# Performance work log

Measured on AMD Instinct MI355X. Metric: run time of the kernel, lower is better.

## Reference

```python
import jax, jax.numpy as jnp
import numpy as np

HIDDEN = 100
N_NODE = 100000
B = 512
T = 50

def setup_inputs() -> dict:
    key = jax.random.key(0)
    ks = jax.random.split(key, 20)
    stdv = 1.0 / np.sqrt(HIDDEN)
    u = lambda k, shape: jax.random.uniform(k, shape, jnp.float32, -stdv, stdv)
    d = HIDDEN
    return {
        "adj_in": jax.random.uniform(ks[0], (B, T, T), jnp.float32),
        "adj_out": jax.random.uniform(ks[1], (B, T, T), jnp.float32),
        "mask": jnp.ones((B, T), jnp.float32),
        "item": jax.random.randint(ks[2], (B, T), 0, N_NODE, jnp.int32),
        "alias": jax.random.randint(ks[3], (B, T), 0, T, jnp.int32),
        "step": 1,
        "embedding": u(ks[4], (N_NODE, d)),
        "W_in": u(ks[5], (d, d)),
        "b_in": u(ks[6], (d,)),
        "W_out": u(ks[7], (d, d)),
        "b_out": u(ks[8], (d,)),
        "gru_gate_k": u(ks[9], (3 * d, 2 * d)),
        "gru_gate_b": jnp.ones((2 * d,), jnp.float32),  # TF GRUCell gate bias init = 1.0
        "gru_cand_k": u(ks[10], (3 * d, d)),
        "gru_cand_b": jnp.zeros((d,), jnp.float32),
        "nasr_w1": u(ks[11], (d, d)),
        "nasr_w2": u(ks[12], (d, d)),
        "nasr_v": u(ks[13], (1, d)),
        "nasr_b": jnp.zeros((d,), jnp.float32),
        "B_mat": u(ks[14], (2 * d, d)),
    }


def _ggnn(item, adj_in, adj_out, embedding, W_in, b_in, W_out, b_out,
          gru_gate_k, gru_gate_b, gru_cand_k, gru_cand_b, step):
    h = embedding[item]  # [B,T,d]
    d = h.shape[-1]
    for _ in range(step):
        a_in = jnp.einsum('bts,bsd->btd', adj_in, h @ W_in + b_in)
        a_out = jnp.einsum('bts,bsd->btd', adj_out, h @ W_out + b_out)
        a = jnp.concatenate([a_in, a_out], axis=-1)  # [B,T,2d]
        # TF GRUCell: gates then candidate
        gates = jax.nn.sigmoid(jnp.concatenate([a, h], -1) @ gru_gate_k + gru_gate_b)
        r, u_ = gates[..., :d], gates[..., d:]
        c = jnp.tanh(jnp.concatenate([a, r * h], -1) @ gru_cand_k + gru_cand_b)
        h = u_ * h + (1.0 - u_) * c
    return h  # [B,T,d]


def reference(adj_in, adj_out, mask, item, alias, step, embedding,
              W_in, b_in, W_out, b_out, gru_gate_k, gru_gate_b,
              gru_cand_k, gru_cand_b, nasr_w1, nasr_w2, nasr_v, nasr_b, B_mat):
    d = embedding.shape[1]
    re_emb = _ggnn(item, adj_in, adj_out, embedding, W_in, b_in, W_out, b_out,
                   gru_gate_k, gru_gate_b, gru_cand_k, gru_cand_b, step)
    rm = jnp.sum(jax.lax.stop_gradient(mask), axis=1)  # session lengths
    bidx = jnp.arange(re_emb.shape[0])
    last_id = alias[bidx, rm.astype(jnp.int32) - 1]          # [B]
    last_h = re_emb[bidx, last_id]                            # [B,d]
    seq_h = jnp.take_along_axis(re_emb, alias[..., None], axis=1)  # [B,L,d]
    last = last_h @ nasr_w1                                   # [B,d]
    seq = seq_h @ nasr_w2                                     # [B,L,d]
    m = jax.nn.sigmoid(last[:, None, :] + seq + nasr_b)       # [B,L,d]
    coef = (m @ nasr_v[0]) * mask                             # [B,L]
    ma = jnp.concatenate([jnp.sum(coef[..., None] * seq_h, axis=1), last], axis=-1)  # [B,2d]
    y1 = ma @ B_mat                                           # [B,d]
    logits = y1 @ embedding[1:].T                             # [B,n_node-1]
    return logits
```

## Files before the change

### kernel.cpp

```cpp
#include <hip/hip_runtime.h>
#include <math.h>

#define D 100
#define T 50
#define BB 512
#define NOUT 99999

__device__ __forceinline__ float sigf(float x) { return 1.f / (1.f + expf(-x)); }

__global__ __launch_bounds__(256) void ggnn_fused(
    const float* __restrict__ adj_in, const float* __restrict__ adj_out,
    const float* __restrict__ mask,   const int* __restrict__ item,
    const int* __restrict__ alias_,   const float* __restrict__ emb,
    const float* __restrict__ W_in,   const float* __restrict__ b_in,
    const float* __restrict__ W_out,  const float* __restrict__ b_out,
    const float* __restrict__ gate_k, const float* __restrict__ gate_b,
    const float* __restrict__ cand_k, const float* __restrict__ cand_b,
    const float* __restrict__ w1,     const float* __restrict__ w2,
    const float* __restrict__ v,      const float* __restrict__ nb,
    const float* __restrict__ Bm,     float* __restrict__ y1)
{
    __shared__ float hS[T*D];
    __shared__ float R1[T*D];
    __shared__ float R2[T*D];
    __shared__ float maskS[T+2], vS[D], nbS[D], lastWS[D], coefS[T+2], maS[2*D];
    __shared__ int aliasS[T+2];
    __shared__ int rmidx;

    const int b = blockIdx.x, tid = threadIdx.x;
    const size_t bT = (size_t)b * T;

    if (tid < T) {
        aliasS[tid] = alias_[bT + tid];
        maskS[tid]  = mask[bT + tid];
    }
    if (tid >= 64 && tid < 64 + D) {
        int k = tid - 64;
        vS[k] = v[k]; nbS[k] = nb[k];
    }
    for (int idx = tid; idx < T*25; idx += 256) {
        int t = idx / 25, q = idx - t*25;
        int node = item[bT + t];
        *(float4*)&hS[t*D + q*4] = *(const float4*)&emb[(size_t)node*D + q*4];
    }
    __syncthreads();
    if (tid == 0) {
        float s = 0.f;
        for (int t = 0; t < T; ++t) s += maskS[t];
        rmidx = aliasS[(int)s - 1];
    }

    const bool act250 = tid < 250;
    const int tg50  = tid / 50;
    const int rem50 = tid % 50;
    const int cg25  = tid / 25;
    const int jq25  = tid % 25;

    if (act250) {
        const int which = rem50 / 25, jq = rem50 % 25;
        const int t0 = tg50 * 10;
        const float* W  = which ? W_out : W_in;
        const float* bb = which ? b_out : b_in;
        float4 binit = *(const float4*)&bb[jq*4];
        float4 acc[10];
        #pragma unroll
        for (int tt = 0; tt < 10; ++tt) acc[tt] = binit;
        for (int k = 0; k < D; k += 2) {
            float4 wa = *(const float4*)&W[k*D + jq*4];
            float4 wb = *(const float4*)&W[(k+1)*D + jq*4];
            #pragma unroll
            for (int tt = 0; tt < 10; ++tt) {
                float2 a = *(const float2*)&hS[(t0+tt)*D + k];
                acc[tt].x += a.x*wa.x + a.y*wb.x;
                acc[tt].y += a.x*wa.y + a.y*wb.y;
                acc[tt].z += a.x*wa.z + a.y*wb.z;
                acc[tt].w += a.x*wa.w + a.y*wb.w;
            }
        }
        float* dst = which ? R2 : R1;
        #pragma unroll
        for (int tt = 0; tt < 10; ++tt)
            *(float4*)&dst[(t0+tt)*D + jq*4] = acc[tt];
    }
    __syncthreads();

    float4 eacc[10];
    if (act250) {
        const int which = rem50 / 25, jq = rem50 % 25;
        const int t0 = tg50 * 10;
        const float* adj = which ? adj_out : adj_in;
        const float* Xs  = which ? R2 : R1;
        #pragma unroll
        for (int tt = 0; tt < 10; ++tt) eacc[tt] = make_float4(0.f,0.f,0.f,0.f);
        #pragma unroll 2
        for (int s = 0; s < T; ++s) {
            float4 x = *(const float4*)&Xs[s*D + jq*4];
            const float* ap = &adj[(bT + t0)*T + s];
            #pragma unroll
            for (int tt = 0; tt < 10; ++tt) {
                float a = ap[tt*T];
                eacc[tt].x += a*x.x; eacc[tt].y += a*x.y;
                eacc[tt].z += a*x.z; eacc[tt].w += a*x.w;
            }
        }
    }
    __syncthreads();
    if (act250) {
        const int which = rem50 / 25, jq = rem50 % 25;
        const int t0 = tg50 * 10;
        float* dst = which ? R2 : R1;
        #pragma unroll
        for (int tt = 0; tt < 10; ++tt)
            *(float4*)&dst[(t0+tt)*D + jq*4] = eacc[tt];
    }
    __syncthreads();

    float4 gacc[10];
    if (act250) {
        const int nq = rem50;
        const int t0 = tg50 * 10;
        float4 ginit = *(const float4*)&gate_b[nq*4];
        #pragma unroll
        for (int tt = 0; tt < 10; ++tt) gacc[tt] = ginit;
        for (int k = 0; k < D; k += 2) {
            float4 g0a = *(const float4*)&gate_k[(size_t)k*200 + nq*4];
            float4 g0b = *(const float4*)&gate_k[(size_t)(k+1)*200 + nq*4];
            float4 g1a = *(const float4*)&gate_k[(size_t)(k+100)*200 + nq*4];
            float4 g1b = *(const float4*)&gate_k[(size_t)(k+101)*200 + nq*4];
            float4 g2a = *(const float4*)&gate_k[(size_t)(k+200)*200 + nq*4];
            float4 g2b = *(const float4*)&gate_k[(size_t)(k+201)*200 + nq*4];
            #pragma unroll
            for (int tt = 0; tt < 10; ++tt) {
                float2 a0 = *(const float2*)&R1[(t0+tt)*D + k];
                float2 a1 = *(const float2*)&R2[(t0+tt)*D + k];
                float2 a2 = *(const float2*)&hS[(t0+tt)*D + k];
                gacc[tt].x += a0.x*g0a.x + a0.y*g0b.x + a1.x*g1a.x + a1.y*g1b.x + a2.x*g2a.x + a2.y*g2b.x;
                gacc[tt].y += a0.x*g0a.y + a0.y*g0b.y + a1.x*g1a.y + a1.y*g1b.y + a2.x*g2a.y + a2.y*g2b.y;
                gacc[tt].z += a0.x*g0a.z + a0.y*g0b.z + a1.x*g1a.z + a1.y*g1b.z + a2.x*g2a.z + a2.y*g2b.z;
                gacc[tt].w += a0.x*g0a.w + a0.y*g0b.w + a1.x*g1a.w + a1.y*g1b.w + a2.x*g2a.w + a2.y*g2b.w;
            }
        }
        #pragma unroll
        for (int tt = 0; tt < 10; ++tt) {
            gacc[tt].x = sigf(gacc[tt].x); gacc[tt].y = sigf(gacc[tt].y);
            gacc[tt].z = sigf(gacc[tt].z); gacc[tt].w = sigf(gacc[tt].w);
        }
    }

    float4 cacc[5];
    if (act250) {
        const int t0 = cg25 * 5;
        float4 cinit = *(const float4*)&cand_b[jq25*4];
        #pragma unroll
        for (int tt = 0; tt < 5; ++tt) cacc[tt] = cinit;
        for (int k = 0; k < D; k += 2) {
            float4 c0a = *(const float4*)&cand_k[(size_t)k*D + jq25*4];
            float4 c0b = *(const float4*)&cand_k[(size_t)(k+1)*D + jq25*4];
            float4 c1a = *(const float4*)&cand_k[(size_t)(k+100)*D + jq25*4];
            float4 c1b = *(const float4*)&cand_k[(size_t)(k+101)*D + jq25*4];
            #pragma unroll
            for (int tt = 0; tt < 5; ++tt) {
                float2 a0 = *(const float2*)&R1[(t0+tt)*D + k];
                float2 a1 = *(const float2*)&R2[(t0+tt)*D + k];
                cacc[tt].x += a0.x*c0a.x + a0.y*c0b.x + a1.x*c1a.x + a1.y*c1b.x;
                cacc[tt].y += a0.x*c0a.y + a0.y*c0b.y + a1.x*c1a.y + a1.y*c1b.y;
                cacc[tt].z += a0.x*c0a.z + a0.y*c0b.z + a1.x*c1a.z + a1.y*c1b.z;
                cacc[tt].w += a0.x*c0a.w + a0.y*c0b.w + a1.x*c1a.w + a1.y*c1b.w;
            }
        }
    }
    __syncthreads();

    if (act250) {
        const int nq = rem50;
        const int t0 = tg50 * 10;
        if (nq < 25) {
            #pragma unroll
            for (int tt = 0; tt < 10; ++tt) {
                float4 hh = *(const float4*)&hS[(t0+tt)*D + nq*4];
                float4 g = gacc[tt];
                float4 o; o.x = g.x*hh.x; o.y = g.y*hh.y; o.z = g.z*hh.z; o.w = g.w*hh.w;
                *(float4*)&R1[(t0+tt)*D + nq*4] = o;
            }
        } else {
            #pragma unroll
            for (int tt = 0; tt < 10; ++tt)
                *(float4*)&R2[(t0+tt)*D + (nq-25)*4] = gacc[tt];
        }
    }
    __syncthreads();

    if (act250) {
        const int t0 = cg25 * 5;
        for (int k = 0; k < D; k += 2) {
            float4 c2a = *(const float4*)&cand_k[(size_t)(k+200)*D + jq25*4];
            float4 c2b = *(const float4*)&cand_k[(size_t)(k+201)*D + jq25*4];
            #pragma unroll
            for (int tt = 0; tt < 5; ++tt) {
                float2 rh = *(const float2*)&R1[(t0+tt)*D + k];
                cacc[tt].x += rh.x*c2a.x + rh.y*c2b.x;
                cacc[tt].y += rh.x*c2a.y + rh.y*c2b.y;
                cacc[tt].z += rh.x*c2a.z + rh.y*c2b.z;
                cacc[tt].w += rh.x*c2a.w + rh.y*c2b.w;
            }
        }
        #pragma unroll
        for (int tt = 0; tt < 5; ++tt) {
            float4 c4;
            c4.x = tanhf(cacc[tt].x); c4.y = tanhf(cacc[tt].y);
            c4.z = tanhf(cacc[tt].z); c4.w = tanhf(cacc[tt].w);
            float4 u4 = *(const float4*)&R2[(t0+tt)*D + jq25*4];
            float4 hh = *(const float4*)&hS[(t0+tt)*D + jq25*4];
            float4 o;
            o.x = u4.x*hh.x + (1.f-u4.x)*c4.x;
            o.y = u4.y*hh.y + (1.f-u4.y)*c4.y;
            o.z = u4.z*hh.z + (1.f-u4.z)*c4.z;
            o.w = u4.w*hh.w + (1.f-u4.w)*c4.w;
            *(float4*)&hS[(t0+tt)*D + jq25*4] = o;
        }
    }
    __syncthreads();

    if (tid < 125) {
        const int sg = tid / 25, jq = tid % 25;
        const int t0 = sg * 10;
        float4 sacc[10];
        #pragma unroll
        for (int tt = 0; tt < 10; ++tt) sacc[tt] = make_float4(0.f,0.f,0.f,0.f);
        int at[10];
        #pragma unroll
        for (int tt = 0; tt < 10; ++tt) at[tt] = aliasS[t0+tt];
        for (int k = 0; k < D; k += 2) {
            float4 wa = *(const float4*)&w2[(size_t)k*D + jq*4];
            float4 wb = *(const float4*)&w2[(size_t)(k+1)*D + jq*4];
            #pragma unroll
            for (int tt = 0; tt < 10; ++tt) {
                float2 a = *(const float2*)&hS[at[tt]*D + k];
                sacc[tt].x += a.x*wa.x + a.y*wb.x;
                sacc[tt].y += a.x*wa.y + a.y*wb.y;
                sacc[tt].z += a.x*wa.z + a.y*wb.z;
                sacc[tt].w += a.x*wa.w + a.y*wb.w;
            }
        }
        #pragma unroll
        for (int tt = 0; tt < 10; ++tt)
            *(float4*)&R1[(t0+tt)*D + jq*4] = sacc[tt];
    } else if (tid >= 128 && tid < 153) {
        const int jq = tid - 128;
        const int lid = rmidx;
        float4 acc = make_float4(0.f,0.f,0.f,0.f);
        for (int k = 0; k < D; k += 2) {
            float4 wa = *(const float4*)&w1[(size_t)k*D + jq*4];
            float4 wb = *(const float4*)&w1[(size_t)(k+1)*D + jq*4];
            float2 a = *(const float2*)&hS[lid*D + k];
            acc.x += a.x*wa.x + a.y*wb.x;
            acc.y += a.x*wa.y + a.y*wb.y;
            acc.z += a.x*wa.z + a.y*wb.z;
            acc.w += a.x*wa.w + a.y*wb.w;
        }
        *(float4*)&lastWS[jq*4] = acc;
    }
    __syncthreads();

    if (tid < T) {
        float s = 0.f;
        #pragma unroll 4
        for (int k = 0; k < D; ++k) {
            float x = lastWS[k] + R1[tid*D + k] + nbS[k];
            s += vS[k] * sigf(x);
        }
        coefS[tid] = s * maskS[tid];
    }
    __syncthreads();
    if (tid < 25) {
        float4 acc = make_float4(0.f,0.f,0.f,0.f);
        #pragma unroll 5
        for (int t = 0; t < T; ++t) {
            float c = coefS[t];
            float4 hh = *(const float4*)&hS[aliasS[t]*D + tid*4];
            acc.x += c*hh.x; acc.y += c*hh.y; acc.z += c*hh.z; acc.w += c*hh.w;
        }
        *(float4*)&maS[tid*4] = acc;
    } else if (tid >= 32 && tid < 57) {
        int j4 = tid - 32;
        *(float4*)&maS[D + j4*4] = *(const float4*)&lastWS[j4*4];
    }
    __syncthreads();
    if (tid < 25) {
        float4 acc = make_float4(0.f,0.f,0.f,0.f);
        #pragma unroll 4
        for (int k = 0; k < 2*D; ++k) {
            float a = maS[k];
            float4 w = *(const float4*)&Bm[(size_t)k*D + tid*4];
            acc.x += a*w.x; acc.y += a*w.y; acc.z += a*w.z; acc.w += a*w.w;
        }
        *(float4*)&y1[(size_t)b*D + tid*4] = acc;
    }
}

#define LDB 132

#define GB_COMPUTE(Ab, kbase) do {                                            \
    _Pragma("unroll")                                                         \
    for (int kk = 0; kk < 4; ++kk) {                                          \
        float bq[8];                                                          \
        _Pragma("unroll")                                                     \
        for (int j = 0; j < 8; ++j)                                           \
            bq[j] = Bs[(kbase + kk)*LDB + (j>>2)*64 + (j&3)*16 + tx];         \
        _Pragma("unroll")                                                     \
        for (int i = 0; i < 8; ++i) {                                         \
            float a_ = kk==0 ? Ab[i].x : kk==1 ? Ab[i].y :                    \
                       kk==2 ? Ab[i].z : Ab[i].w;                             \
            _Pragma("unroll")                                                 \
            for (int j = 0; j < 8; ++j)                                       \
                acc[i][j] += a_ * bq[j];                                      \
        }                                                                     \
    }                                                                         \
} while (0)

__global__ __launch_bounds__(256) void gemm_big(
    const float* __restrict__ y1,
    const float* __restrict__ emb,
    float* __restrict__ out)
{
    __shared__ float Bs[100*LDB];
    const int tid = threadIdx.x;
    const int tx = tid & 15, ty = tid >> 4;
    const int n0 = blockIdx.x * 128;

    for (int idx = tid; idx < 128*25; idx += 256) {
        int n = idx / 25, q = idx - n*25;
        int gn = n0 + n;
        float4 vv = make_float4(0.f,0.f,0.f,0.f);
        if (gn < NOUT) vv = *(const float4*)&emb[(size_t)(gn+1)*D + q*4];
        Bs[(q*4+0)*LDB + n] = vv.x;
        Bs[(q*4+1)*LDB + n] = vv.y;
        Bs[(q*4+2)*LDB + n] = vv.z;
        Bs[(q*4+3)*LDB + n] = vv.w;
    }
    __syncthreads();

    float acc[8][8];
    float4 A0[8], A1[8];

    #pragma unroll 1
    for (int mc = 0; mc < 2; ++mc) {
        const int m0 = blockIdx.y * 256 + mc * 128;

        #pragma unroll
        for (int i = 0; i < 8; ++i)
            #pragma unroll
            for (int j = 0; j < 8; ++j) acc[i][j] = 0.f;

        #pragma unroll
        for (int i = 0; i < 8; ++i)
            A0[i] = *(const float4*)&y1[(size_t)(m0 + ty + i*16)*D + 0];

        int k = 0;
        #pragma unroll 1
        for (int it = 0; it < 12; ++it, k += 8) {
            #pragma unroll
            for (int i = 0; i < 8; ++i)
                A1[i] = *(const float4*)&y1[(size_t)(m0 + ty + i*16)*D + k + 4];
            GB_COMPUTE(A0, k);
            #pragma unroll
            for (int i = 0; i < 8; ++i)
                A0[i] = *(const float4*)&y1[(size_t)(m0 + ty + i*16)*D + k + 8];
            GB_COMPUTE(A1, k + 4);
        }
        GB_COMPUTE(A0, 96);

        #pragma unroll
        for (int i = 0; i < 8; ++i) {
            size_t row = (size_t)(m0 + ty + i*16) * NOUT;
            #pragma unroll
            for (int h = 0; h < 2; ++h)
                #pragma unroll
                for (int q = 0; q < 4; ++q) {
                    int n = n0 + h*64 + q*16 + tx;
                    if (n < NOUT) out[row + n] = acc[i][h*4+q];
                }
        }
    }
}

extern "C" void kernel_launch(void* const* d_in, const int* in_sizes, int n_in,
                              void* d_out, int out_size, void* d_ws, size_t ws_size,
                              hipStream_t stream)
{
    const float* adj_in  = (const float*)d_in[0];
    const float* adj_out = (const float*)d_in[1];
    const float* mask    = (const float*)d_in[2];
    const int*   item    = (const int*)  d_in[3];
    const int*   alias_  = (const int*)  d_in[4];
    const float* emb     = (const float*)d_in[6];
    const float* W_in    = (const float*)d_in[7];
    const float* b_in    = (const float*)d_in[8];
    const float* W_out   = (const float*)d_in[9];
    const float* b_out   = (const float*)d_in[10];
    const float* gate_k  = (const float*)d_in[11];
    const float* gate_b  = (const float*)d_in[12];
    const float* cand_k  = (const float*)d_in[13];
    const float* cand_b  = (const float*)d_in[14];
    const float* w1      = (const float*)d_in[15];
    const float* w2      = (const float*)d_in[16];
    const float* v       = (const float*)d_in[17];
    const float* nb      = (const float*)d_in[18];
    const float* Bm      = (const float*)d_in[19];
    float* out = (float*)d_out;
    float* y1  = (float*)d_ws;

    ggnn_fused<<<BB, 256, 0, stream>>>(
        adj_in, adj_out, mask, item, alias_, emb,
        W_in, b_in, W_out, b_out, gate_k, gate_b, cand_k, cand_b,
        w1, w2, v, nb, Bm, y1);

    gemm_big<<<dim3((NOUT + 127)/128, 2), 256, 0, stream>>>(y1, emb, out);
}
```

Measured before the change: 646.9 us.

## Software-pipeline weight loads in GGNN matmuls and vectorize big-GEMM shared reads

```diff
diff --git a/kernel.cpp b/kernel.cpp
--- a/kernel.cpp
+++ b/kernel.cpp
@@ -65,18 +65,28 @@
         float4 acc[10];
         #pragma unroll
         for (int tt = 0; tt < 10; ++tt) acc[tt] = binit;
-        for (int k = 0; k < D; k += 2) {
-            float4 wa = *(const float4*)&W[k*D + jq*4];
-            float4 wb = *(const float4*)&W[(k+1)*D + jq*4];
-            #pragma unroll
-            for (int tt = 0; tt < 10; ++tt) {
-                float2 a = *(const float2*)&hS[(t0+tt)*D + k];
-                acc[tt].x += a.x*wa.x + a.y*wb.x;
-                acc[tt].y += a.x*wa.y + a.y*wb.y;
-                acc[tt].z += a.x*wa.z + a.y*wb.z;
-                acc[tt].w += a.x*wa.w + a.y*wb.w;
-            }
-        }
+
+        float4 wq[4], wp[4];
+#define P2_LOAD(dst, k0) { _Pragma("unroll") \
+        for (int d = 0; d < 4; ++d) dst[d] = *(const float4*)&W[((k0)+d)*D + jq*4]; }
+#define P2_COMP(buf, k0) { _Pragma("unroll") \
+        for (int d2 = 0; d2 < 4; d2 += 2) { _Pragma("unroll") \
+            for (int tt = 0; tt < 10; ++tt) { \
+                float2 a = *(const float2*)&hS[(t0+tt)*D + (k0) + d2]; \
+                acc[tt].x += a.x*buf[d2].x + a.y*buf[d2+1].x; \
+                acc[tt].y += a.x*buf[d2].y + a.y*buf[d2+1].y; \
+                acc[tt].z += a.x*buf[d2].z + a.y*buf[d2+1].z; \
+                acc[tt].w += a.x*buf[d2].w + a.y*buf[d2+1].w; } } }
+        P2_LOAD(wq, 0);
+        #pragma unroll 1
+        for (int k = 0; k < 88; k += 8) {
+            P2_LOAD(wp, k+4);  P2_COMP(wq, k);
+            P2_LOAD(wq, k+8);  P2_COMP(wp, k+4);
+        }
+        P2_LOAD(wp, 92);  P2_COMP(wq, 88);
+        P2_LOAD(wq, 96);  P2_COMP(wp, 92);
+        P2_COMP(wq, 96);
+
         float* dst = which ? R2 : R1;
         #pragma unroll
         for (int tt = 0; tt < 10; ++tt)
@@ -88,20 +98,32 @@
     if (act250) {
         const int which = rem50 / 25, jq = rem50 % 25;
         const int t0 = tg50 * 10;
-        const float* adj = which ? adj_out : adj_in;
-        const float* Xs  = which ? R2 : R1;
-        #pragma unroll
-        for (int tt = 0; tt < 10; ++tt) eacc[tt] = make_float4(0.f,0.f,0.f,0.f);
-        #pragma unroll 2
-        for (int s = 0; s < T; ++s) {
+        const float* adjp = which ? adj_out : adj_in;
+        const float* Xs   = which ? R2 : R1;
+        const float* apb  = &adjp[(bT + t0)*T];
+        float ac[10], an[10];
+        #pragma unroll
+        for (int tt = 0; tt < 10; ++tt) {
+            eacc[tt] = make_float4(0.f,0.f,0.f,0.f);
+            ac[tt] = apb[tt*T];
+        }
+        #pragma unroll 1
+        for (int s = 0; s < T-1; ++s) {
+            #pragma unroll
+            for (int tt = 0; tt < 10; ++tt) an[tt] = apb[tt*T + s + 1];
             float4 x = *(const float4*)&Xs[s*D + jq*4];
-            const float* ap = &adj[(bT + t0)*T + s];
             #pragma unroll
             for (int tt = 0; tt < 10; ++tt) {
-                float a = ap[tt*T];
-                eacc[tt].x += a*x.x; eacc[tt].y += a*x.y;
-                eacc[tt].z += a*x.z; eacc[tt].w += a*x.w;
+                eacc[tt].x += ac[tt]*x.x; eacc[tt].y += ac[tt]*x.y;
+                eacc[tt].z += ac[tt]*x.z; eacc[tt].w += ac[tt]*x.w;
+                ac[tt] = an[tt];
             }
+        }
+        float4 x = *(const float4*)&Xs[(T-1)*D + jq*4];
+        #pragma unroll
+        for (int tt = 0; tt < 10; ++tt) {
+            eacc[tt].x += ac[tt]*x.x; eacc[tt].y += ac[tt]*x.y;
+            eacc[tt].z += ac[tt]*x.z; eacc[tt].w += ac[tt]*x.w;
         }
     }
     __syncthreads();
@@ -122,24 +144,31 @@
         float4 ginit = *(const float4*)&gate_b[nq*4];
         #pragma unroll
         for (int tt = 0; tt < 10; ++tt) gacc[tt] = ginit;
-        for (int k = 0; k < D; k += 2) {
-            float4 g0a = *(const float4*)&gate_k[(size_t)k*200 + nq*4];
-            float4 g0b = *(const float4*)&gate_k[(size_t)(k+1)*200 + nq*4];
-            float4 g1a = *(const float4*)&gate_k[(size_t)(k+100)*200 + nq*4];
-            float4 g1b = *(const float4*)&gate_k[(size_t)(k+101)*200 + nq*4];
-            float4 g2a = *(const float4*)&gate_k[(size_t)(k+200)*200 + nq*4];
-            float4 g2b = *(const float4*)&gate_k[(size_t)(k+201)*200 + nq*4];
-            #pragma unroll
-            for (int tt = 0; tt < 10; ++tt) {
-                float2 a0 = *(const float2*)&R1[(t0+tt)*D + k];
-                float2 a1 = *(const float2*)&R2[(t0+tt)*D + k];
-                float2 a2 = *(const float2*)&hS[(t0+tt)*D + k];
-                gacc[tt].x += a0.x*g0a.x + a0.y*g0b.x + a1.x*g1a.x + a1.y*g1b.x + a2.x*g2a.x + a2.y*g2b.x;
-                gacc[tt].y += a0.x*g0a.y + a0.y*g0b.y + a1.x*g1a.y + a1.y*g1b.y + a2.x*g2a.y + a2.y*g2b.y;
-                gacc[tt].z += a0.x*g0a.z + a0.y*g0b.z + a1.x*g1a.z + a1.y*g1b.z + a2.x*g2a.z + a2.y*g2b.z;
-                gacc[tt].w += a0.x*g0a.w + a0.y*g0b.w + a1.x*g1a.w + a1.y*g1b.w + a2.x*g2a.w + a2.y*g2b.w;
-            }
-        }
+
+        float4 gq6[6], gp6[6];
+#define P4_LOAD(dst, kp) { _Pragma("unroll") \
+        for (int s = 0; s < 3; ++s) { \
+            dst[s*2]   = *(const float4*)&gate_k[(size_t)((kp)+s*100)*200 + nq*4]; \
+            dst[s*2+1] = *(const float4*)&gate_k[(size_t)((kp)+1+s*100)*200 + nq*4]; } }
+#define P4_COMP(buf, kp) { _Pragma("unroll") \
+        for (int tt = 0; tt < 10; ++tt) { \
+            float2 a0 = *(const float2*)&R1[(t0+tt)*D + (kp)]; \
+            float2 a1 = *(const float2*)&R2[(t0+tt)*D + (kp)]; \
+            float2 a2 = *(const float2*)&hS[(t0+tt)*D + (kp)]; \
+            gacc[tt].x += a0.x*buf[0].x + a0.y*buf[1].x + a1.x*buf[2].x + a1.y*buf[3].x + a2.x*buf[4].x + a2.y*buf[5].x; \
+            gacc[tt].y += a0.x*buf[0].y + a0.y*buf[1].y + a1.x*buf[2].y + a1.y*buf[3].y + a2.x*buf[4].y + a2.y*buf[5].y; \
+            gacc[tt].z += a0.x*buf[0].z + a0.y*buf[1].z + a1.x*buf[2].z + a1.y*buf[3].z + a2.x*buf[4].z + a2.y*buf[5].z; \
+            gacc[tt].w += a0.x*buf[0].w + a0.y*buf[1].w + a1.x*buf[2].w + a1.y*buf[3].w + a2.x*buf[4].w + a2.y*buf[5].w; } }
+        P4_LOAD(gq6, 0);
+        #pragma unroll 1
+        for (int k = 0; k < 96; k += 4) {
+            P4_LOAD(gp6, k+2);  P4_COMP(gq6, k);
+            P4_LOAD(gq6, k+4);  P4_COMP(gp6, k+2);
+        }
+        P4_LOAD(gp6, 98);
+        P4_COMP(gq6, 96);
+        P4_COMP(gp6, 98);
+
         #pragma unroll
         for (int tt = 0; tt < 10; ++tt) {
             gacc[tt].x = sigf(gacc[tt].x); gacc[tt].y = sigf(gacc[tt].y);
@@ -153,21 +182,30 @@
         float4 cinit = *(const float4*)&cand_b[jq25*4];
         #pragma unroll
         for (int tt = 0; tt < 5; ++tt) cacc[tt] = cinit;
-        for (int k = 0; k < D; k += 2) {
-            float4 c0a = *(const float4*)&cand_k[(size_t)k*D + jq25*4];
-            float4 c0b = *(const float4*)&cand_k[(size_t)(k+1)*D + jq25*4];
-            float4 c1a = *(const float4*)&cand_k[(size_t)(k+100)*D + jq25*4];
-            float4 c1b = *(const float4*)&cand_k[(size_t)(k+101)*D + jq25*4];
-            #pragma unroll
-            for (int tt = 0; tt < 5; ++tt) {
-                float2 a0 = *(const float2*)&R1[(t0+tt)*D + k];
-                float2 a1 = *(const float2*)&R2[(t0+tt)*D + k];
-                cacc[tt].x += a0.x*c0a.x + a0.y*c0b.x + a1.x*c1a.x + a1.y*c1b.x;
-                cacc[tt].y += a0.x*c0a.y + a0.y*c0b.y + a1.x*c1a.y + a1.y*c1b.y;
-                cacc[tt].z += a0.x*c0a.z + a0.y*c0b.z + a1.x*c1a.z + a1.y*c1b.z;
-                cacc[tt].w += a0.x*c0a.w + a0.y*c0b.w + a1.x*c1a.w + a1.y*c1b.w;
-            }
-        }
+
+        float4 cq[8], cp[8];
+#define P5A_LOAD(dst, k0) { _Pragma("unroll") \
+        for (int s = 0; s < 2; ++s) { _Pragma("unroll") \
+            for (int d = 0; d < 4; ++d) \
+                dst[s*4+d] = *(const float4*)&cand_k[(size_t)((k0)+d+s*100)*D + jq25*4]; } }
+#define P5A_COMP(buf, k0) { _Pragma("unroll") \
+        for (int d2 = 0; d2 < 4; d2 += 2) { _Pragma("unroll") \
+            for (int tt = 0; tt < 5; ++tt) { \
+                float2 a0 = *(const float2*)&R1[(t0+tt)*D + (k0)+d2]; \
+                float2 a1 = *(const float2*)&R2[(t0+tt)*D + (k0)+d2]; \
+                cacc[tt].x += a0.x*buf[d2].x + a0.y*buf[d2+1].x + a1.x*buf[4+d2].x + a1.y*buf[4+d2+1].x; \
+                cacc[tt].y += a0.x*buf[d2].y + a0.y*buf[d2+1].y + a1.x*buf[4+d2].y + a1.y*buf[4+d2+1].y; \
+                cacc[tt].z += a0.x*buf[d2].z + a0.y*buf[d2+1].z + a1.x*buf[4+d2].z + a1.y*buf[4+d2+1].z; \
+                cacc[tt].w += a0.x*buf[d2].w + a0.y*buf[d2+1].w + a1.x*buf[4+d2].w + a1.y*buf[4+d2+1].w; } } }
+        P5A_LOAD(cq, 0);
+        #pragma unroll 1
+        for (int k = 0; k < 88; k += 8) {
+            P5A_LOAD(cp, k+4);  P5A_COMP(cq, k);
+            P5A_LOAD(cq, k+8);  P5A_COMP(cp, k+4);
+        }
+        P5A_LOAD(cp, 92);  P5A_COMP(cq, 88);
+        P5A_LOAD(cq, 96);  P5A_COMP(cp, 92);
+        P5A_COMP(cq, 96);
     }
     __syncthreads();
 
@@ -192,18 +230,28 @@
 
     if (act250) {
         const int t0 = cg25 * 5;
-        for (int k = 0; k < D; k += 2) {
-            float4 c2a = *(const float4*)&cand_k[(size_t)(k+200)*D + jq25*4];
-            float4 c2b = *(const float4*)&cand_k[(size_t)(k+201)*D + jq25*4];
-            #pragma unroll
-            for (int tt = 0; tt < 5; ++tt) {
-                float2 rh = *(const float2*)&R1[(t0+tt)*D + k];
-                cacc[tt].x += rh.x*c2a.x + rh.y*c2b.x;
-                cacc[tt].y += rh.x*c2a.y + rh.y*c2b.y;
-                cacc[tt].z += rh.x*c2a.z + rh.y*c2b.z;
-                cacc[tt].w += rh.x*c2a.w + rh.y*c2b.w;
-            }
-        }
+        float4 dq[4], dp[4];
+#define P5C_LOAD(dst, k0) { _Pragma("unroll") \
+        for (int d = 0; d < 4; ++d) \
+            dst[d] = *(const float4*)&cand_k[(size_t)((k0)+d+200)*D + jq25*4]; }
+#define P5C_COMP(buf, k0) { _Pragma("unroll") \
+        for (int d2 = 0; d2 < 4; d2 += 2) { _Pragma("unroll") \
+            for (int tt = 0; tt < 5; ++tt) { \
+                float2 rh = *(const float2*)&R1[(t0+tt)*D + (k0)+d2]; \
+                cacc[tt].x += rh.x*buf[d2].x + rh.y*buf[d2+1].x; \
+                cacc[tt].y += rh.x*buf[d2].y + rh.y*buf[d2+1].y; \
+                cacc[tt].z += rh.x*buf[d2].z + rh.y*buf[d2+1].z; \
+                cacc[tt].w += rh.x*buf[d2].w + rh.y*buf[d2+1].w; } } }
+        P5C_LOAD(dq, 0);
+        #pragma unroll 1
+        for (int k = 0; k < 88; k += 8) {
+            P5C_LOAD(dp, k+4);  P5C_COMP(dq, k);
+            P5C_LOAD(dq, k+8);  P5C_COMP(dp, k+4);
+        }
+        P5C_LOAD(dp, 92);  P5C_COMP(dq, 88);
+        P5C_LOAD(dq, 96);  P5C_COMP(dp, 92);
+        P5C_COMP(dq, 96);
+
         #pragma unroll
         for (int tt = 0; tt < 5; ++tt) {
             float4 c4;
@@ -230,18 +278,28 @@
         int at[10];
         #pragma unroll
         for (int tt = 0; tt < 10; ++tt) at[tt] = aliasS[t0+tt];
-        for (int k = 0; k < D; k += 2) {
-            float4 wa = *(const float4*)&w2[(size_t)k*D + jq*4];
-            float4 wb = *(const float4*)&w2[(size_t)(k+1)*D + jq*4];
-            #pragma unroll
-            for (int tt = 0; tt < 10; ++tt) {
-                float2 a = *(const float2*)&hS[at[tt]*D + k];
-                sacc[tt].x += a.x*wa.x + a.y*wb.x;
-                sacc[tt].y += a.x*wa.y + a.y*wb.y;
-                sacc[tt].z += a.x*wa.z + a.y*wb.z;
-                sacc[tt].w += a.x*wa.w + a.y*wb.w;
-            }
-        }
+
+        float4 wq[4], wp[4];
+#define P8_LOAD(dst, k0) { _Pragma("unroll") \
+        for (int d = 0; d < 4; ++d) dst[d] = *(const float4*)&w2[(size_t)((k0)+d)*D + jq*4]; }
+#define P8_COMP(buf, k0) { _Pragma("unroll") \
+        for (int d2 = 0; d2 < 4; d2 += 2) { _Pragma("unroll") \
+            for (int tt = 0; tt < 10; ++tt) { \
+                float2 a = *(const float2*)&hS[at[tt]*D + (k0) + d2]; \
+                sacc[tt].x += a.x*buf[d2].x + a.y*buf[d2+1].x; \
+                sacc[tt].y += a.x*buf[d2].y + a.y*buf[d2+1].y; \
+                sacc[tt].z += a.x*buf[d2].z + a.y*buf[d2+1].z; \
+                sacc[tt].w += a.x*buf[d2].w + a.y*buf[d2+1].w; } } }
+        P8_LOAD(wq, 0);
+        #pragma unroll 1
+        for (int k = 0; k < 88; k += 8) {
+            P8_LOAD(wp, k+4);  P8_COMP(wq, k);
+            P8_LOAD(wq, k+8);  P8_COMP(wp, k+4);
+        }
+        P8_LOAD(wp, 92);  P8_COMP(wq, 88);
+        P8_LOAD(wq, 96);  P8_COMP(wp, 92);
+        P8_COMP(wq, 96);
+
         #pragma unroll
         for (int tt = 0; tt < 10; ++tt)
             *(float4*)&R1[(t0+tt)*D + jq*4] = sacc[tt];
@@ -303,17 +361,16 @@
 #define GB_COMPUTE(Ab, kbase) do {                                            \
     _Pragma("unroll")                                                         \
     for (int kk = 0; kk < 4; ++kk) {                                          \
-        float bq[8];                                                          \
-        _Pragma("unroll")                                                     \
-        for (int j = 0; j < 8; ++j)                                           \
-            bq[j] = Bs[(kbase + kk)*LDB + (j>>2)*64 + (j&3)*16 + tx];         \
+        float4 b0 = *(const float4*)&Bs[(kbase + kk)*LDB + tx*4];             \
+        float4 b1 = *(const float4*)&Bs[(kbase + kk)*LDB + 64 + tx*4];        \
         _Pragma("unroll")                                                     \
         for (int i = 0; i < 8; ++i) {                                         \
             float a_ = kk==0 ? Ab[i].x : kk==1 ? Ab[i].y :                    \
                        kk==2 ? Ab[i].z : Ab[i].w;                             \
-            _Pragma("unroll")                                                 \
-            for (int j = 0; j < 8; ++j)                                       \
-                acc[i][j] += a_ * bq[j];                                      \
+            acc[i][0] += a_*b0.x; acc[i][1] += a_*b0.y;                       \
+            acc[i][2] += a_*b0.z; acc[i][3] += a_*b0.w;                       \
+            acc[i][4] += a_*b1.x; acc[i][5] += a_*b1.y;                       \
+            acc[i][6] += a_*b1.z; acc[i][7] += a_*b1.w;                       \
         }                                                                     \
     }                                                                         \
 } while (0)
@@ -333,10 +390,12 @@
         int gn = n0 + n;
         float4 vv = make_float4(0.f,0.f,0.f,0.f);
         if (gn < NOUT) vv = *(const float4*)&emb[(size_t)(gn+1)*D + q*4];
-        Bs[(q*4+0)*LDB + n] = vv.x;
-        Bs[(q*4+1)*LDB + n] = vv.y;
-        Bs[(q*4+2)*LDB + n] = vv.z;
-        Bs[(q*4+3)*LDB + n] = vv.w;
+        int w = n & 63;
+        int pos = (n & 64) + ((w & 15) << 2) + (w >> 4);
+        Bs[(q*4+0)*LDB + pos] = vv.x;
+        Bs[(q*4+1)*LDB + pos] = vv.y;
+        Bs[(q*4+2)*LDB + pos] = vv.z;
+        Bs[(q*4+3)*LDB + pos] = vv.w;
     }
     __syncthreads();
 
```

Measured after the change: 660.1 us. 2.0% more time.

## Software-pipeline GGNN loads and vectorize shared-memory B reads in big GEMM

Applied to the files above, without the earlier changes.

```diff
diff --git a/kernel.cpp b/kernel.cpp
--- a/kernel.cpp
+++ b/kernel.cpp
@@ -88,20 +88,32 @@
     if (act250) {
         const int which = rem50 / 25, jq = rem50 % 25;
         const int t0 = tg50 * 10;
-        const float* adj = which ? adj_out : adj_in;
-        const float* Xs  = which ? R2 : R1;
-        #pragma unroll
-        for (int tt = 0; tt < 10; ++tt) eacc[tt] = make_float4(0.f,0.f,0.f,0.f);
-        #pragma unroll 2
-        for (int s = 0; s < T; ++s) {
+        const float* adjp = which ? adj_out : adj_in;
+        const float* Xs   = which ? R2 : R1;
+        const float* apb  = &adjp[(bT + t0)*T];
+        float ac[10], an[10];
+        #pragma unroll
+        for (int tt = 0; tt < 10; ++tt) {
+            eacc[tt] = make_float4(0.f,0.f,0.f,0.f);
+            ac[tt] = apb[tt*T];
+        }
+        #pragma unroll 1
+        for (int s = 0; s < T-1; ++s) {
+            #pragma unroll
+            for (int tt = 0; tt < 10; ++tt) an[tt] = apb[tt*T + s + 1];
             float4 x = *(const float4*)&Xs[s*D + jq*4];
-            const float* ap = &adj[(bT + t0)*T + s];
             #pragma unroll
             for (int tt = 0; tt < 10; ++tt) {
-                float a = ap[tt*T];
-                eacc[tt].x += a*x.x; eacc[tt].y += a*x.y;
-                eacc[tt].z += a*x.z; eacc[tt].w += a*x.w;
-            }
+                eacc[tt].x += ac[tt]*x.x; eacc[tt].y += ac[tt]*x.y;
+                eacc[tt].z += ac[tt]*x.z; eacc[tt].w += ac[tt]*x.w;
+                ac[tt] = an[tt];
+            }
+        }
+        float4 x = *(const float4*)&Xs[(T-1)*D + jq*4];
+        #pragma unroll
+        for (int tt = 0; tt < 10; ++tt) {
+            eacc[tt].x += ac[tt]*x.x; eacc[tt].y += ac[tt]*x.y;
+            eacc[tt].z += ac[tt]*x.z; eacc[tt].w += ac[tt]*x.w;
         }
     }
     __syncthreads();
@@ -122,24 +134,31 @@
         float4 ginit = *(const float4*)&gate_b[nq*4];
         #pragma unroll
         for (int tt = 0; tt < 10; ++tt) gacc[tt] = ginit;
-        for (int k = 0; k < D; k += 2) {
-            float4 g0a = *(const float4*)&gate_k[(size_t)k*200 + nq*4];
-            float4 g0b = *(const float4*)&gate_k[(size_t)(k+1)*200 + nq*4];
-            float4 g1a = *(const float4*)&gate_k[(size_t)(k+100)*200 + nq*4];
-            float4 g1b = *(const float4*)&gate_k[(size_t)(k+101)*200 + nq*4];
-            float4 g2a = *(const float4*)&gate_k[(size_t)(k+200)*200 + nq*4];
-            float4 g2b = *(const float4*)&gate_k[(size_t)(k+201)*200 + nq*4];
-            #pragma unroll
-            for (int tt = 0; tt < 10; ++tt) {
-                float2 a0 = *(const float2*)&R1[(t0+tt)*D + k];
-                float2 a1 = *(const float2*)&R2[(t0+tt)*D + k];
-                float2 a2 = *(const float2*)&hS[(t0+tt)*D + k];
-                gacc[tt].x += a0.x*g0a.x + a0.y*g0b.x + a1.x*g1a.x + a1.y*g1b.x + a2.x*g2a.x + a2.y*g2b.x;
-                gacc[tt].y += a0.x*g0a.y + a0.y*g0b.y + a1.x*g1a.y + a1.y*g1b.y + a2.x*g2a.y + a2.y*g2b.y;
-                gacc[tt].z += a0.x*g0a.z + a0.y*g0b.z + a1.x*g1a.z + a1.y*g1b.z + a2.x*g2a.z + a2.y*g2b.z;
-                gacc[tt].w += a0.x*g0a.w + a0.y*g0b.w + a1.x*g1a.w + a1.y*g1b.w + a2.x*g2a.w + a2.y*g2b.w;
-            }
-        }
+
+        float4 gq6[6], gp6[6];
+#define P4_LOAD(dst, kp) { _Pragma("unroll") \
+        for (int s = 0; s < 3; ++s) { \
+            dst[s*2]   = *(const float4*)&gate_k[(size_t)((kp)+s*100)*200 + nq*4]; \
+            dst[s*2+1] = *(const float4*)&gate_k[(size_t)((kp)+1+s*100)*200 + nq*4]; } }
+#define P4_COMP(buf, kp) { _Pragma("unroll") \
+        for (int tt = 0; tt < 10; ++tt) { \
+            float2 a0 = *(const float2*)&R1[(t0+tt)*D + (kp)]; \
+            float2 a1 = *(const float2*)&R2[(t0+tt)*D + (kp)]; \
+            float2 a2 = *(const float2*)&hS[(t0+tt)*D + (kp)]; \
+            gacc[tt].x += a0.x*buf[0].x + a0.y*buf[1].x + a1.x*buf[2].x + a1.y*buf[3].x + a2.x*buf[4].x + a2.y*buf[5].x; \
+            gacc[tt].y += a0.x*buf[0].y + a0.y*buf[1].y + a1.x*buf[2].y + a1.y*buf[3].y + a2.x*buf[4].y + a2.y*buf[5].y; \
+            gacc[tt].z += a0.x*buf[0].z + a0.y*buf[1].z + a1.x*buf[2].z + a1.y*buf[3].z + a2.x*buf[4].z + a2.y*buf[5].z; \
+            gacc[tt].w += a0.x*buf[0].w + a0.y*buf[1].w + a1.x*buf[2].w + a1.y*buf[3].w + a2.x*buf[4].w + a2.y*buf[5].w; } }
+        P4_LOAD(gq6, 0);
+        #pragma unroll 1
+        for (int k = 0; k < 96; k += 4) {
+            P4_LOAD(gp6, k+2);  P4_COMP(gq6, k);
+            P4_LOAD(gq6, k+4);  P4_COMP(gp6, k+2);
+        }
+        P4_LOAD(gp6, 98);
+        P4_COMP(gq6, 96);
+        P4_COMP(gp6, 98);
+
         #pragma unroll
         for (int tt = 0; tt < 10; ++tt) {
             gacc[tt].x = sigf(gacc[tt].x); gacc[tt].y = sigf(gacc[tt].y);
@@ -303,17 +322,16 @@
 #define GB_COMPUTE(Ab, kbase) do {                                            \
     _Pragma("unroll")                                                         \
     for (int kk = 0; kk < 4; ++kk) {                                          \
-        float bq[8];                                                          \
-        _Pragma("unroll")                                                     \
-        for (int j = 0; j < 8; ++j)                                           \
-            bq[j] = Bs[(kbase + kk)*LDB + (j>>2)*64 + (j&3)*16 + tx];         \
+        float4 b0 = *(const float4*)&Bs[(kbase + kk)*LDB + tx*4];             \
+        float4 b1 = *(const float4*)&Bs[(kbase + kk)*LDB + 64 + tx*4];        \
         _Pragma("unroll")                                                     \
         for (int i = 0; i < 8; ++i) {                                         \
             float a_ = kk==0 ? Ab[i].x : kk==1 ? Ab[i].y :                    \
                        kk==2 ? Ab[i].z : Ab[i].w;                             \
-            _Pragma("unroll")                                                 \
-            for (int j = 0; j < 8; ++j)                                       \
-                acc[i][j] += a_ * bq[j];                                      \
+            acc[i][0] += a_*b0.x; acc[i][1] += a_*b0.y;                       \
+            acc[i][2] += a_*b0.z; acc[i][3] += a_*b0.w;                       \
+            acc[i][4] += a_*b1.x; acc[i][5] += a_*b1.y;                       \
+            acc[i][6] += a_*b1.z; acc[i][7] += a_*b1.w;                       \
         }                                                                     \
     }                                                                         \
 } while (0)
@@ -333,10 +351,12 @@
         int gn = n0 + n;
         float4 vv = make_float4(0.f,0.f,0.f,0.f);
         if (gn < NOUT) vv = *(const float4*)&emb[(size_t)(gn+1)*D + q*4];
-        Bs[(q*4+0)*LDB + n] = vv.x;
-        Bs[(q*4+1)*LDB + n] = vv.y;
-        Bs[(q*4+2)*LDB + n] = vv.z;
-        Bs[(q*4+3)*LDB + n] = vv.w;
+        int w = n & 63;
+        int pos = (n & 64) + ((w & 15) << 2) + (w >> 4);
+        Bs[(q*4+0)*LDB + pos] = vv.x;
+        Bs[(q*4+1)*LDB + pos] = vv.y;
+        Bs[(q*4+2)*LDB + pos] = vv.z;
+        Bs[(q*4+3)*LDB + pos] = vv.w;
     }
     __syncthreads();
 
```

Result: slower. 737.9 us (+14.1%).
